# Kernel optimization log

Hardware: AMD Instinct MI355X
Metric: run time of the kernel (lower is better)

## Reference

```python
import jax, jax.numpy as jnp
import numpy as np

# Module config (matches init_kwargs)
T = 16384          # tokens
D = 4096           # input_dim
E = 256            # num_experts
G = 8              # num_expert_group
EPG = E // G       # experts_per_group = 32
TOPK_GROUP = 2     # topk within each group
TOP_K = 8          # total selected experts per token
NSEL = TOP_K // TOPK_GROUP  # num_selected_groups = 4


def setup_inputs() -> dict:
    key = jax.random.key(0)
    k1, k2 = jax.random.split(key)
    x = jax.random.normal(k1, (T, D), dtype=jnp.float32)
    # gate weight, nn.Linear(D, E, bias=False) -> W: [E, D]
    W = jax.random.normal(k2, (E, D), dtype=jnp.float32) * (1.0 / np.sqrt(D))
    return {"x": x, "W": W}


def reference(x, W):
    # logits -> softmax probs over all experts
    probs = jax.nn.softmax(x @ W.T, axis=-1)                 # [T, E]
    scores_grouped = probs.reshape(-1, G, EPG)               # [T, G, EPG]

    # per-group top-(topk_group) expert scores; group score = their sum
    gvals, gids_local = jax.lax.top_k(scores_grouped, TOPK_GROUP)  # [T, G, tg]
    group_scores = gvals.sum(axis=-1)                        # [T, G]

    # select best groups
    _, sel_groups = jax.lax.top_k(group_scores, NSEL)        # [T, NSEL]

    # gather the per-group local top ids for the selected groups
    local = jnp.take_along_axis(gids_local, sel_groups[:, :, None], axis=1)  # [T, NSEL, tg]
    # global expert ids; reshape order matches torch loop (g outer, k inner)
    topk_ids = (sel_groups[:, :, None] * EPG + local).reshape(-1, TOP_K)     # [T, top_k]

    # gather candidate probs and renormalize
    cand_probs = jnp.take_along_axis(probs, topk_ids, axis=-1)               # [T, top_k]
    topk_weights = cand_probs / (cand_probs.sum(axis=-1, keepdims=True) + 1e-9)

    # aux load-balancing loss from top-1 expert usage
    top1 = topk_ids[:, 0]                                    # [T]
    expert_usage = jnp.zeros((E,), probs.dtype).at[top1].add(1.0) / x.shape[0]
    aux_loss = E * (expert_usage * probs.mean(axis=0)).sum()

    return topk_weights, topk_ids, aux_loss
```

## Files before the change

kernel.cpp:

```cpp
#include <hip/hip_runtime.h>
#include <hip/hip_bf16.h>
#include <stdint.h>

#define T_TOK 16384
#define D_DIM 4096
#define E_EXP 256

typedef __attribute__((ext_vector_type(8))) short bf16x8;
typedef __attribute__((ext_vector_type(4))) float f32x4;

__device__ __forceinline__ uint32_t bf16_rne(float f) {
    uint32_t u = __float_as_uint(f);
    return (u + 0x7FFFu + ((u >> 16) & 1u)) >> 16;
}

__global__ __launch_bounds__(256)
void wsplit_kernel(const float* __restrict__ W, uint16_t* __restrict__ Wh,
                   uint16_t* __restrict__ Wm, uint16_t* __restrict__ Wl,
                   float* __restrict__ acc512) {
    const int idx = blockIdx.x * 256 + threadIdx.x;
    const float4 v = ((const float4*)W)[idx];
    const float f[4] = {v.x, v.y, v.z, v.w};
    uint32_t h[4], m[4], l[4];
    #pragma unroll
    for (int j = 0; j < 4; ++j) {
        h[j] = bf16_rne(f[j]);
        const float r1 = f[j] - __uint_as_float(h[j] << 16);
        m[j] = bf16_rne(r1);
        const float r2 = r1 - __uint_as_float(m[j] << 16);
        l[j] = bf16_rne(r2);
    }
    ((uint2*)Wh)[idx] = make_uint2(h[0] | (h[1] << 16), h[2] | (h[3] << 16));
    ((uint2*)Wm)[idx] = make_uint2(m[0] | (m[1] << 16), m[2] | (m[3] << 16));
    ((uint2*)Wl)[idx] = make_uint2(l[0] | (l[1] << 16), l[2] | (l[3] << 16));
    if (blockIdx.x == 0) {
        acc512[threadIdx.x] = 0.0f;
        acc512[threadIdx.x + 256] = 0.0f;
    }
}

#define LDK 72

#define LOADB(bh, bm, bl, ko) do { \
    _Pragma("unroll") \
    for (int nt = 0; nt < 2; ++nt) { \
        const uint32_t o = woff[nt] + (uint32_t)(ko); \
        bh[nt] = *(const bf16x8*)(Wh + o); \
        bm[nt] = *(const bf16x8*)(Wm + o); \
        bl[nt] = *(const bf16x8*)(Wl + o); \
    } } while (0)

#define SPLIT_STORE(buf) do { \
    const float f[8] = {p0.x, p0.y, p0.z, p0.w, p1.x, p1.y, p1.z, p1.w}; \
    uint32_t h[8], m[8], l[8]; \
    _Pragma("unroll") \
    for (int j = 0; j < 8; ++j) { \
        h[j] = bf16_rne(f[j]); \
        const float r1 = f[j] - __uint_as_float(h[j] << 16); \
        m[j] = bf16_rne(r1); \
        const float r2 = r1 - __uint_as_float(m[j] << 16); \
        l[j] = bf16_rne(r2); \
    } \
    uint4 hv, mv, lv; \
    hv.x = h[0] | (h[1] << 16); hv.y = h[2] | (h[3] << 16); \
    hv.z = h[4] | (h[5] << 16); hv.w = h[6] | (h[7] << 16); \
    mv.x = m[0] | (m[1] << 16); mv.y = m[2] | (m[3] << 16); \
    mv.z = m[4] | (m[5] << 16); mv.w = m[6] | (m[7] << 16); \
    lv.x = l[0] | (l[1] << 16); lv.y = l[2] | (l[3] << 16); \
    lv.z = l[4] | (l[5] << 16); lv.w = l[6] | (l[7] << 16); \
    *(uint4*)&sXh[buf][swoff] = hv; \
    *(uint4*)&sXm[buf][swoff] = mv; \
    *(uint4*)&sXl[buf][swoff] = lv; \
} while (0)

#define COMPUTE(buf, s, bh, bm, bl) do { \
    bf16x8 ah[4], am[4], al[4]; \
    _Pragma("unroll") \
    for (int mt = 0; mt < 4; ++mt) { \
        const int ro = (mt * 16 + l16) * LDK + (s) * 32 + quad * 8; \
        ah[mt] = *(const bf16x8*)&sXh[buf][ro]; \
        am[mt] = *(const bf16x8*)&sXm[buf][ro]; \
        al[mt] = *(const bf16x8*)&sXl[buf][ro]; \
    } \
    _Pragma("unroll") \
    for (int mt = 0; mt < 4; ++mt) \
        _Pragma("unroll") \
        for (int nt = 0; nt < 2; ++nt) \
            acc[mt][nt] = __builtin_amdgcn_mfma_f32_16x16x32_bf16(ah[mt], bh[nt], acc[mt][nt], 0, 0, 0); \
    _Pragma("unroll") \
    for (int mt = 0; mt < 4; ++mt) \
        _Pragma("unroll") \
        for (int nt = 0; nt < 2; ++nt) \
            acc[mt][nt] = __builtin_amdgcn_mfma_f32_16x16x32_bf16(ah[mt], bm[nt], acc[mt][nt], 0, 0, 0); \
    _Pragma("unroll") \
    for (int mt = 0; mt < 4; ++mt) \
        _Pragma("unroll") \
        for (int nt = 0; nt < 2; ++nt) \
            acc[mt][nt] = __builtin_amdgcn_mfma_f32_16x16x32_bf16(am[mt], bh[nt], acc[mt][nt], 0, 0, 0); \
    _Pragma("unroll") \
    for (int mt = 0; mt < 4; ++mt) \
        _Pragma("unroll") \
        for (int nt = 0; nt < 2; ++nt) \
            acc[mt][nt] = __builtin_amdgcn_mfma_f32_16x16x32_bf16(am[mt], bm[nt], acc[mt][nt], 0, 0, 0); \
    _Pragma("unroll") \
    for (int mt = 0; mt < 4; ++mt) \
        _Pragma("unroll") \
        for (int nt = 0; nt < 2; ++nt) \
            acc[mt][nt] = __builtin_amdgcn_mfma_f32_16x16x32_bf16(ah[mt], bl[nt], acc[mt][nt], 0, 0, 0); \
    _Pragma("unroll") \
    for (int mt = 0; mt < 4; ++mt) \
        _Pragma("unroll") \
        for (int nt = 0; nt < 2; ++nt) \
            acc[mt][nt] = __builtin_amdgcn_mfma_f32_16x16x32_bf16(al[mt], bh[nt], acc[mt][nt], 0, 0, 0); \
} while (0)

__global__ __launch_bounds__(512, 2)
void gemm_kernel(const float* __restrict__ x, const uint16_t* __restrict__ Wh,
                 const uint16_t* __restrict__ Wm, const uint16_t* __restrict__ Wl,
                 float* __restrict__ logits) {
    __shared__ uint16_t sXh[2][64 * LDK];
    __shared__ uint16_t sXm[2][64 * LDK];
    __shared__ uint16_t sXl[2][64 * LDK];
    const int t = threadIdx.x;
    const int tok0 = blockIdx.x * 64;
    const int wave = t >> 6, lane = t & 63;
    const int quad = lane >> 4, l16 = lane & 15;

    const int stok = t >> 3;
    const int skoff = (t & 7) * 8;
    const float* xp = x + (size_t)(tok0 + stok) * D_DIM + skoff;
    const int swoff = stok * LDK + skoff;

    uint32_t woff[2];
    #pragma unroll
    for (int nt = 0; nt < 2; ++nt)
        woff[nt] = (uint32_t)(wave * 32 + nt * 16 + l16) * D_DIM + quad * 8;

    const f32x4 zf = {0.f, 0.f, 0.f, 0.f};
    f32x4 acc[4][2];
    #pragma unroll
    for (int mt = 0; mt < 4; ++mt)
        #pragma unroll
        for (int nt = 0; nt < 2; ++nt) acc[mt][nt] = zf;

    float4 p0 = ((const float4*)xp)[0];
    float4 p1 = ((const float4*)xp)[1];
    bf16x8 cbh[2], cbm[2], cbl[2], nbh[2], nbm[2], nbl[2];

    SPLIT_STORE(0);
    LOADB(cbh, cbm, cbl, 0);
    {
        const float* xn = xp + 64;
        p0 = ((const float4*)xn)[0];
        p1 = ((const float4*)xn)[1];
    }
    __syncthreads();

    for (int kb = 0; kb < D_DIM; kb += 64) {
        const int cur = (kb >> 6) & 1;
        LOADB(nbh, nbm, nbl, kb + 32);
        COMPUTE(cur, 0, cbh, cbm, cbl);
        if (kb + 64 < D_DIM) {
            LOADB(cbh, cbm, cbl, kb + 64);
            SPLIT_STORE(cur ^ 1);
        }
        if (kb + 128 < D_DIM) {
            const float* xn = xp + kb + 128;
            p0 = ((const float4*)xn)[0];
            p1 = ((const float4*)xn)[1];
        }
        COMPUTE(cur, 1, nbh, nbm, nbl);
        __syncthreads();
    }

    #pragma unroll
    for (int mt = 0; mt < 4; ++mt)
        #pragma unroll
        for (int nt = 0; nt < 2; ++nt)
            #pragma unroll
            for (int r = 0; r < 4; ++r)
                logits[(size_t)(tok0 + mt * 16 + quad * 4 + r) * E_EXP +
                       wave * 32 + nt * 16 + l16] = acc[mt][nt][r];
}

__device__ __forceinline__ float wave_max(float v) {
    #pragma unroll
    for (int off = 32; off >= 1; off >>= 1)
        v = fmaxf(v, __shfl_xor(v, off, 64));
    return v;
}
__device__ __forceinline__ float wave_sum(float v) {
    #pragma unroll
    for (int off = 32; off >= 1; off >>= 1)
        v += __shfl_xor(v, off, 64);
    return v;
}

#define TOKS_PER_WAVE 4

__global__ __launch_bounds__(256)
void router_kernel(const float* __restrict__ logits,
                   float* __restrict__ out_w,
                   float* __restrict__ out_id,
                   float* __restrict__ g_psum,
                   float* __restrict__ g_cnt) {
    __shared__ float lds_psum[E_EXP];
    __shared__ float lds_cnt[E_EXP];
    const int t = threadIdx.x;
    lds_psum[t] = 0.0f; lds_cnt[t] = 0.0f;
    __syncthreads();

    const int wave = t >> 6;
    const int lane = t & 63;
    const int tok0 = blockIdx.x * (4 * TOKS_PER_WAVE) + wave * TOKS_PER_WAVE;

    float r0 = 0.f, r1 = 0.f, r2 = 0.f, r3 = 0.f;

    for (int it = 0; it < TOKS_PER_WAVE; ++it) {
        const int tok = tok0 + it;
        const float4 lg = *(const float4*)(logits + (size_t)tok * E_EXP + lane * 4);

        const float M = wave_max(fmaxf(fmaxf(lg.x, lg.y), fmaxf(lg.z, lg.w)));
        float p0 = __expf(lg.x - M);
        float p1 = __expf(lg.y - M);
        float p2 = __expf(lg.z - M);
        float p3 = __expf(lg.w - M);
        const float inv = 1.0f / wave_sum(p0 + p1 + p2 + p3);
        p0 *= inv; p1 *= inv; p2 *= inv; p3 *= inv;
        r0 += p0; r1 += p1; r2 += p2; r3 += p3;

        const int e0 = lane * 4;
        float v1 = p0, v2 = p1; int i1 = e0, i2 = e0 + 1;
        if (p1 > p0) { v1 = p1; i1 = e0 + 1; v2 = p0; i2 = e0; }
        if (p2 > v1)      { v2 = v1; i2 = i1; v1 = p2; i1 = e0 + 2; }
        else if (p2 > v2) { v2 = p2; i2 = e0 + 2; }
        if (p3 > v1)      { v2 = v1; i2 = i1; v1 = p3; i1 = e0 + 3; }
        else if (p3 > v2) { v2 = p3; i2 = e0 + 3; }

        #pragma unroll
        for (int off = 1; off <= 4; off <<= 1) {
            const float ov1 = __shfl_xor(v1, off, 64);
            const int   oi1 = __shfl_xor(i1, off, 64);
            const float ov2 = __shfl_xor(v2, off, 64);
            const int   oi2 = __shfl_xor(i2, off, 64);
            float n1, n2; int ni1, ni2;
            const bool o_first = (ov1 > v1) || (ov1 == v1 && oi1 < i1);
            if (o_first) {
                n1 = ov1; ni1 = oi1;
                const bool s = (ov2 > v1) || (ov2 == v1 && oi2 < i1);
                n2 = s ? ov2 : v1; ni2 = s ? oi2 : i1;
            } else {
                n1 = v1; ni1 = i1;
                const bool s = (ov1 > v2) || (ov1 == v2 && oi1 < i2);
                n2 = s ? ov1 : v2; ni2 = s ? oi1 : i2;
            }
            v1 = n1; i1 = ni1; v2 = n2; i2 = ni2;
        }

        float gv1[8], gv2[8], gsc[8]; int gi1[8], gi2[8];
        #pragma unroll
        for (int g = 0; g < 8; ++g) {
            gv1[g] = __shfl(v1, g * 8, 64);
            gv2[g] = __shfl(v2, g * 8, 64);
            gi1[g] = __shfl(i1, g * 8, 64);
            gi2[g] = __shfl(i2, g * 8, 64);
            gsc[g] = gv1[g] + gv2[g];
        }

        float cp[8]; int cid[8];
        int usedmask = 0;
        #pragma unroll
        for (int r = 0; r < 4; ++r) {
            float best = -1.0f; int bg = 0;
            float b1 = 0.f, b2 = 0.f; int bi1 = 0, bi2 = 0;
            #pragma unroll
            for (int g = 0; g < 8; ++g) {
                const bool ok = (((usedmask >> g) & 1) == 0) && (gsc[g] > best);
                if (ok) { best = gsc[g]; bg = g;
                          b1 = gv1[g]; b2 = gv2[g]; bi1 = gi1[g]; bi2 = gi2[g]; }
            }
            usedmask |= (1 << bg);
            cp[2 * r] = b1; cp[2 * r + 1] = b2;
            cid[2 * r] = bi1; cid[2 * r + 1] = bi2;
        }

        float wsum = 1e-9f;
        #pragma unroll
        for (int j = 0; j < 8; ++j) wsum += cp[j];
        const float winv = 1.0f / wsum;

        if (lane == 0) {
            #pragma unroll
            for (int j = 0; j < 8; ++j) {
                out_w[(size_t)tok * 8 + j] = cp[j] * winv;
                out_id[(size_t)tok * 8 + j] = (float)cid[j];
            }
            atomicAdd(&lds_cnt[cid[0]], 1.0f);
        }
    }

    atomicAdd(&lds_psum[lane * 4 + 0], r0);
    atomicAdd(&lds_psum[lane * 4 + 1], r1);
    atomicAdd(&lds_psum[lane * 4 + 2], r2);
    atomicAdd(&lds_psum[lane * 4 + 3], r3);
    __syncthreads();
    atomicAdd(&g_psum[t], lds_psum[t]);
    atomicAdd(&g_cnt[t], lds_cnt[t]);
}

__global__ __launch_bounds__(256)
void aux_kernel(const float* __restrict__ g_psum, const float* __restrict__ g_cnt,
                float* __restrict__ out_aux) {
    __shared__ float red[E_EXP];
    const int t = threadIdx.x;
    const float invT = 1.0f / (float)T_TOK;
    red[t] = (g_cnt[t] * invT) * (g_psum[t] * invT);
    __syncthreads();
    #pragma unroll
    for (int s = 128; s > 0; s >>= 1) {
        if (t < s) red[t] += red[t + s];
        __syncthreads();
    }
    if (t == 0) out_aux[0] = (float)E_EXP * red[0];
}

extern "C" void kernel_launch(void* const* d_in, const int* in_sizes, int n_in,
                              void* d_out, int out_size, void* d_ws, size_t ws_size,
                              hipStream_t stream) {
    const float* x = (const float*)d_in[0];
    const float* W = (const float*)d_in[1];

    float* out = (float*)d_out;
    float* out_w = out;
    float* out_id = out + T_TOK * 8;
    float* out_aux = out + 2 * T_TOK * 8;

    float* g_psum = (float*)d_ws;
    float* g_cnt = g_psum + E_EXP;
    float* logits = g_psum + 512;
    uint16_t* Wh = (uint16_t*)(logits + (size_t)T_TOK * E_EXP);
    uint16_t* Wm = Wh + (size_t)E_EXP * D_DIM;
    uint16_t* Wl = Wm + (size_t)E_EXP * D_DIM;

    wsplit_kernel<<<1024, 256, 0, stream>>>(W, Wh, Wm, Wl, g_psum);
    gemm_kernel<<<T_TOK / 64, 512, 0, stream>>>(x, Wh, Wm, Wl, logits);
    router_kernel<<<T_TOK / (4 * TOKS_PER_WAVE), 256, 0, stream>>>(
        logits, out_w, out_id, g_psum, g_cnt);
    aux_kernel<<<1, 256, 0, stream>>>(g_psum, g_cnt, out_aux);
}
```

Measured before the change: 575.8 us.

## Fuse softmax/grouped top-k router into GEMM epilogue via shared-memory logits

The router stage moves into the GEMM kernel's epilogue. Accumulators are staged in 32-token halves into shared memory that reuses the X-tile pool, then each wave runs softmax, grouped top-k, renormalization and the aux partial sums directly. This removes the global logits buffer write and re-read and one kernel launch. Global count atomics are also skipped when a block's count is zero. The trade-offs are more register pressure in a kernel launched with (512,2) bounds, which could cause spills, plus extra block-level syncs in the epilogue.

```diff
diff --git a/kernel.cpp b/kernel.cpp
--- a/kernel.cpp
+++ b/kernel.cpp
@@ -40,6 +40,7 @@
 }
 
 #define LDK 72
+#define SROW 272
 
 #define LOADB(bh, bm, bl, ko) do { \
     _Pragma("unroll") \
@@ -68,19 +69,19 @@
     mv.z = m[4] | (m[5] << 16); mv.w = m[6] | (m[7] << 16); \
     lv.x = l[0] | (l[1] << 16); lv.y = l[2] | (l[3] << 16); \
     lv.z = l[4] | (l[5] << 16); lv.w = l[6] | (l[7] << 16); \
-    *(uint4*)&sXh[buf][swoff] = hv; \
-    *(uint4*)&sXm[buf][swoff] = mv; \
-    *(uint4*)&sXl[buf][swoff] = lv; \
+    *(uint4*)&sXh[(buf) * 4608 + swoff] = hv; \
+    *(uint4*)&sXm[(buf) * 4608 + swoff] = mv; \
+    *(uint4*)&sXl[(buf) * 4608 + swoff] = lv; \
 } while (0)
 
 #define COMPUTE(buf, s, bh, bm, bl) do { \
     bf16x8 ah[4], am[4], al[4]; \
     _Pragma("unroll") \
     for (int mt = 0; mt < 4; ++mt) { \
-        const int ro = (mt * 16 + l16) * LDK + (s) * 32 + quad * 8; \
-        ah[mt] = *(const bf16x8*)&sXh[buf][ro]; \
-        am[mt] = *(const bf16x8*)&sXm[buf][ro]; \
-        al[mt] = *(const bf16x8*)&sXl[buf][ro]; \
+        const int ro = (buf) * 4608 + (mt * 16 + l16) * LDK + (s) * 32 + quad * 8; \
+        ah[mt] = *(const bf16x8*)&sXh[ro]; \
+        am[mt] = *(const bf16x8*)&sXm[ro]; \
+        al[mt] = *(const bf16x8*)&sXl[ro]; \
     } \
     _Pragma("unroll") \
     for (int mt = 0; mt < 4; ++mt) \
@@ -115,12 +116,22 @@
 } while (0)
 
 __global__ __launch_bounds__(512, 2)
-void gemm_kernel(const float* __restrict__ x, const uint16_t* __restrict__ Wh,
-                 const uint16_t* __restrict__ Wm, const uint16_t* __restrict__ Wl,
-                 float* __restrict__ logits) {
-    __shared__ uint16_t sXh[2][64 * LDK];
-    __shared__ uint16_t sXm[2][64 * LDK];
-    __shared__ uint16_t sXl[2][64 * LDK];
+void gemm_router_kernel(const float* __restrict__ x,
+                        const uint16_t* __restrict__ Wh,
+                        const uint16_t* __restrict__ Wm,
+                        const uint16_t* __restrict__ Wl,
+                        float* __restrict__ out_w,
+                        float* __restrict__ out_id,
+                        float* __restrict__ g_psum,
+                        float* __restrict__ g_cnt) {
+    __shared__ __align__(16) char pool[55296];
+    uint16_t* sXh = (uint16_t*)pool;
+    uint16_t* sXm = (uint16_t*)(pool + 18432);
+    uint16_t* sXl = (uint16_t*)(pool + 36864);
+    float* sLog = (float*)pool;
+    float* lds_psum = (float*)(pool + 34816);
+    float* lds_cnt = (float*)(pool + 35840);
+
     const int t = threadIdx.x;
     const int tok0 = blockIdx.x * 64;
     const int wave = t >> 6, lane = t & 63;
@@ -173,130 +184,114 @@
         __syncthreads();
     }
 
-    #pragma unroll
-    for (int mt = 0; mt < 4; ++mt)
+    if (t < 256) { lds_psum[t] = 0.0f; lds_cnt[t] = 0.0f; }
+
+    float r0 = 0.f, r1 = 0.f, r2 = 0.f, r3 = 0.f;
+
+    #pragma unroll
+    for (int hh = 0; hh < 2; ++hh) {
         #pragma unroll
-        for (int nt = 0; nt < 2; ++nt)
-            #pragma unroll
-            for (int r = 0; r < 4; ++r)
-                logits[(size_t)(tok0 + mt * 16 + quad * 4 + r) * E_EXP +
-                       wave * 32 + nt * 16 + l16] = acc[mt][nt][r];
-}
-
-__device__ __forceinline__ float wave_max(float v) {
-    #pragma unroll
-    for (int off = 32; off >= 1; off >>= 1)
-        v = fmaxf(v, __shfl_xor(v, off, 64));
-    return v;
-}
-__device__ __forceinline__ float wave_sum(float v) {
-    #pragma unroll
-    for (int off = 32; off >= 1; off >>= 1)
-        v += __shfl_xor(v, off, 64);
-    return v;
-}
-
-#define TOKS_PER_WAVE 4
-
-__global__ __launch_bounds__(256)
-void router_kernel(const float* __restrict__ logits,
-                   float* __restrict__ out_w,
-                   float* __restrict__ out_id,
-                   float* __restrict__ g_psum,
-                   float* __restrict__ g_cnt) {
-    __shared__ float lds_psum[E_EXP];
-    __shared__ float lds_cnt[E_EXP];
-    const int t = threadIdx.x;
-    lds_psum[t] = 0.0f; lds_cnt[t] = 0.0f;
-    __syncthreads();
-
-    const int wave = t >> 6;
-    const int lane = t & 63;
-    const int tok0 = blockIdx.x * (4 * TOKS_PER_WAVE) + wave * TOKS_PER_WAVE;
-
-    float r0 = 0.f, r1 = 0.f, r2 = 0.f, r3 = 0.f;
-
-    for (int it = 0; it < TOKS_PER_WAVE; ++it) {
-        const int tok = tok0 + it;
-        const float4 lg = *(const float4*)(logits + (size_t)tok * E_EXP + lane * 4);
-
-        const float M = wave_max(fmaxf(fmaxf(lg.x, lg.y), fmaxf(lg.z, lg.w)));
-        float p0 = __expf(lg.x - M);
-        float p1 = __expf(lg.y - M);
-        float p2 = __expf(lg.z - M);
-        float p3 = __expf(lg.w - M);
-        const float inv = 1.0f / wave_sum(p0 + p1 + p2 + p3);
-        p0 *= inv; p1 *= inv; p2 *= inv; p3 *= inv;
-        r0 += p0; r1 += p1; r2 += p2; r3 += p3;
-
-        const int e0 = lane * 4;
-        float v1 = p0, v2 = p1; int i1 = e0, i2 = e0 + 1;
-        if (p1 > p0) { v1 = p1; i1 = e0 + 1; v2 = p0; i2 = e0; }
-        if (p2 > v1)      { v2 = v1; i2 = i1; v1 = p2; i1 = e0 + 2; }
-        else if (p2 > v2) { v2 = p2; i2 = e0 + 2; }
-        if (p3 > v1)      { v2 = v1; i2 = i1; v1 = p3; i1 = e0 + 3; }
-        else if (p3 > v2) { v2 = p3; i2 = e0 + 3; }
+        for (int u = 0; u < 2; ++u)
+            #pragma unroll
+            for (int nt = 0; nt < 2; ++nt)
+                #pragma unroll
+                for (int r = 0; r < 4; ++r)
+                    sLog[(u * 16 + quad * 4 + r) * SROW + wave * 32 + nt * 16 + l16] =
+                        acc[hh * 2 + u][nt][r];
+        __syncthreads();
 
         #pragma unroll
-        for (int off = 1; off <= 4; off <<= 1) {
-            const float ov1 = __shfl_xor(v1, off, 64);
-            const int   oi1 = __shfl_xor(i1, off, 64);
-            const float ov2 = __shfl_xor(v2, off, 64);
-            const int   oi2 = __shfl_xor(i2, off, 64);
-            float n1, n2; int ni1, ni2;
-            const bool o_first = (ov1 > v1) || (ov1 == v1 && oi1 < i1);
-            if (o_first) {
-                n1 = ov1; ni1 = oi1;
-                const bool s = (ov2 > v1) || (ov2 == v1 && oi2 < i1);
-                n2 = s ? ov2 : v1; ni2 = s ? oi2 : i1;
-            } else {
-                n1 = v1; ni1 = i1;
-                const bool s = (ov1 > v2) || (ov1 == v2 && oi1 < i2);
-                n2 = s ? ov1 : v2; ni2 = s ? oi1 : i2;
+        for (int it = 0; it < 4; ++it) {
+            const int lrow = wave * 4 + it;
+            const int tok = tok0 + hh * 32 + lrow;
+            const float4 lg = *(const float4*)&sLog[lrow * SROW + lane * 4];
+
+            float mx = fmaxf(fmaxf(lg.x, lg.y), fmaxf(lg.z, lg.w));
+            #pragma unroll
+            for (int off = 32; off >= 1; off >>= 1)
+                mx = fmaxf(mx, __shfl_xor(mx, off, 64));
+            float p0_ = __expf(lg.x - mx);
+            float p1_ = __expf(lg.y - mx);
+            float p2_ = __expf(lg.z - mx);
+            float p3_ = __expf(lg.w - mx);
+            float sm = p0_ + p1_ + p2_ + p3_;
+            #pragma unroll
+            for (int off = 32; off >= 1; off >>= 1)
+                sm += __shfl_xor(sm, off, 64);
+            const float inv = 1.0f / sm;
+            p0_ *= inv; p1_ *= inv; p2_ *= inv; p3_ *= inv;
+            r0 += p0_; r1 += p1_; r2 += p2_; r3 += p3_;
+
+            const int e0 = lane * 4;
+            float v1 = p0_, v2 = p1_; int i1 = e0, i2 = e0 + 1;
+            if (p1_ > p0_) { v1 = p1_; i1 = e0 + 1; v2 = p0_; i2 = e0; }
+            if (p2_ > v1)      { v2 = v1; i2 = i1; v1 = p2_; i1 = e0 + 2; }
+            else if (p2_ > v2) { v2 = p2_; i2 = e0 + 2; }
+            if (p3_ > v1)      { v2 = v1; i2 = i1; v1 = p3_; i1 = e0 + 3; }
+            else if (p3_ > v2) { v2 = p3_; i2 = e0 + 3; }
+
+            #pragma unroll
+            for (int off = 1; off <= 4; off <<= 1) {
+                const float ov1 = __shfl_xor(v1, off, 64);
+                const int   oi1 = __shfl_xor(i1, off, 64);
+                const float ov2 = __shfl_xor(v2, off, 64);
+                const int   oi2 = __shfl_xor(i2, off, 64);
+                float n1, n2; int ni1, ni2;
+                const bool o_first = (ov1 > v1) || (ov1 == v1 && oi1 < i1);
+                if (o_first) {
+                    n1 = ov1; ni1 = oi1;
+                    const bool s = (ov2 > v1) || (ov2 == v1 && oi2 < i1);
+                    n2 = s ? ov2 : v1; ni2 = s ? oi2 : i1;
+                } else {
+                    n1 = v1; ni1 = i1;
+                    const bool s = (ov1 > v2) || (ov1 == v2 && oi1 < i2);
+                    n2 = s ? ov1 : v2; ni2 = s ? oi1 : i2;
+                }
+                v1 = n1; i1 = ni1; v2 = n2; i2 = ni2;
             }
-            v1 = n1; i1 = ni1; v2 = n2; i2 = ni2;
+
+            float gv1[8], gv2[8], gsc[8]; int gi1[8], gi2[8];
+            #pragma unroll
+            for (int g = 0; g < 8; ++g) {
+                gv1[g] = __shfl(v1, g * 8, 64);
+                gv2[g] = __shfl(v2, g * 8, 64);
+                gi1[g] = __shfl(i1, g * 8, 64);
+                gi2[g] = __shfl(i2, g * 8, 64);
+                gsc[g] = gv1[g] + gv2[g];
+            }
+
+            float cp[8]; int cid[8];
+            int usedmask = 0;
+            #pragma unroll
+            for (int r = 0; r < 4; ++r) {
+                float best = -1.0f; int bg = 0;
+                float b1 = 0.f, b2 = 0.f; int bi1 = 0, bi2 = 0;
+                #pragma unroll
+                for (int g = 0; g < 8; ++g) {
+                    const bool ok = (((usedmask >> g) & 1) == 0) && (gsc[g] > best);
+                    if (ok) { best = gsc[g]; bg = g;
+                              b1 = gv1[g]; b2 = gv2[g]; bi1 = gi1[g]; bi2 = gi2[g]; }
+                }
+                usedmask |= (1 << bg);
+                cp[2 * r] = b1; cp[2 * r + 1] = b2;
+                cid[2 * r] = bi1; cid[2 * r + 1] = bi2;
+            }
+
+            float wsum = 1e-9f;
+            #pragma unroll
+            for (int j = 0; j < 8; ++j) wsum += cp[j];
+            const float winv = 1.0f / wsum;
+
+            if (lane == 0) {
+                #pragma unroll
+                for (int j = 0; j < 8; ++j) {
+                    out_w[(size_t)tok * 8 + j] = cp[j] * winv;
+                    out_id[(size_t)tok * 8 + j] = (float)cid[j];
+                }
+                atomicAdd(&lds_cnt[cid[0]], 1.0f);
+            }
         }
-
-        float gv1[8], gv2[8], gsc[8]; int gi1[8], gi2[8];
-        #pragma unroll
-        for (int g = 0; g < 8; ++g) {
-            gv1[g] = __shfl(v1, g * 8, 64);
-            gv2[g] = __shfl(v2, g * 8, 64);
-            gi1[g] = __shfl(i1, g * 8, 64);
-            gi2[g] = __shfl(i2, g * 8, 64);
-            gsc[g] = gv1[g] + gv2[g];
-        }
-
-        float cp[8]; int cid[8];
-        int usedmask = 0;
-        #pragma unroll
-        for (int r = 0; r < 4; ++r) {
-            float best = -1.0f; int bg = 0;
-            float b1 = 0.f, b2 = 0.f; int bi1 = 0, bi2 = 0;
-            #pragma unroll
-            for (int g = 0; g < 8; ++g) {
-                const bool ok = (((usedmask >> g) & 1) == 0) && (gsc[g] > best);
-                if (ok) { best = gsc[g]; bg = g;
-                          b1 = gv1[g]; b2 = gv2[g]; bi1 = gi1[g]; bi2 = gi2[g]; }
-            }
-            usedmask |= (1 << bg);
-            cp[2 * r] = b1; cp[2 * r + 1] = b2;
-            cid[2 * r] = bi1; cid[2 * r + 1] = bi2;
-        }
-
-        float wsum = 1e-9f;
-        #pragma unroll
-        for (int j = 0; j < 8; ++j) wsum += cp[j];
-        const float winv = 1.0f / wsum;
-
-        if (lane == 0) {
-            #pragma unroll
-            for (int j = 0; j < 8; ++j) {
-                out_w[(size_t)tok * 8 + j] = cp[j] * winv;
-                out_id[(size_t)tok * 8 + j] = (float)cid[j];
-            }
-            atomicAdd(&lds_cnt[cid[0]], 1.0f);
-        }
+        __syncthreads();
     }
 
     atomicAdd(&lds_psum[lane * 4 + 0], r0);
@@ -304,8 +299,11 @@
     atomicAdd(&lds_psum[lane * 4 + 2], r2);
     atomicAdd(&lds_psum[lane * 4 + 3], r3);
     __syncthreads();
-    atomicAdd(&g_psum[t], lds_psum[t]);
-    atomicAdd(&g_cnt[t], lds_cnt[t]);
+    if (t < 256) {
+        atomicAdd(&g_psum[t], lds_psum[t]);
+        const float c = lds_cnt[t];
+        if (c != 0.0f) atomicAdd(&g_cnt[t], c);
+    }
 }
 
 __global__ __launch_bounds__(256)
@@ -337,14 +335,12 @@
 
     float* g_psum = (float*)d_ws;
     float* g_cnt = g_psum + E_EXP;
-    float* logits = g_psum + 512;
-    uint16_t* Wh = (uint16_t*)(logits + (size_t)T_TOK * E_EXP);
+    uint16_t* Wh = (uint16_t*)(g_psum + 512);
     uint16_t* Wm = Wh + (size_t)E_EXP * D_DIM;
     uint16_t* Wl = Wm + (size_t)E_EXP * D_DIM;
 
     wsplit_kernel<<<1024, 256, 0, stream>>>(W, Wh, Wm, Wl, g_psum);
-    gemm_kernel<<<T_TOK / 64, 512, 0, stream>>>(x, Wh, Wm, Wl, logits);
-    router_kernel<<<T_TOK / (4 * TOKS_PER_WAVE), 256, 0, stream>>>(
-        logits, out_w, out_id, g_psum, g_cnt);
+    gemm_router_kernel<<<T_TOK / 64, 512, 0, stream>>>(
+        x, Wh, Wm, Wl, out_w, out_id, g_psum, g_cnt);
     aux_kernel<<<1, 256, 0, stream>>>(g_psum, g_cnt, out_aux);
 }
```

After: 564.9 us. No clear change (-1.9%).
